# Kernel tuning notes

Measured on AMD Instinct MI355X. Metric: run time of the kernel, lower is better.

Reference implementation:

```python
import jax, jax.numpy as jnp
import numpy as np

K = 3
PAD = 1
K2 = K * K


def _deform_conv(x, offset, w, b):
    """torchvision-style DeformConv2d, stride=1, padding=1, kernel=3, dilation=1.
    x: [B,C,H,W]; offset: [B,2*K2,H,W] (per-tap (dy,dx) interleaved); w: [O,C,K,K]; b: [O].
    """
    B, C, H, W = x.shape
    # kernel tap offsets relative to center (padding=1 => taps at -1,0,1)
    ky = (jnp.arange(K) - PAD).astype(x.dtype)
    kx = (jnp.arange(K) - PAD).astype(x.dtype)
    ky = jnp.repeat(ky, K)   # [K2]
    kx = jnp.tile(kx, K)     # [K2]

    off = offset.reshape(B, K2, 2, H, W)
    # sampling coordinates: [B,K2,H,W]
    yy = off[:, :, 0] + ky[None, :, None, None] + jnp.arange(H, dtype=x.dtype)[None, None, :, None]
    xx = off[:, :, 1] + kx[None, :, None, None] + jnp.arange(W, dtype=x.dtype)[None, None, None, :]

    def sample_one(img, yb, xb):  # img [C,H,W]; yb,xb [K2,H,W]
        y0 = jnp.floor(yb)
        x0 = jnp.floor(xb)
        dy = yb - y0
        dx = xb - x0
        y0i = y0.astype(jnp.int32)
        x0i = x0.astype(jnp.int32)
        img_flat = img.reshape(C, -1)

        def gather(yi, xi):
            valid = (yi >= 0) & (yi < H) & (xi >= 0) & (xi < W)
            idx = jnp.clip(yi, 0, H - 1) * W + jnp.clip(xi, 0, W - 1)
            v = jnp.take(img_flat, idx.reshape(-1), axis=1).reshape(C, K2, H, W)
            return v * valid[None].astype(img.dtype)

        v00 = gather(y0i, x0i)
        v01 = gather(y0i, x0i + 1)
        v10 = gather(y0i + 1, x0i)
        v11 = gather(y0i + 1, x0i + 1)
        w00 = ((1 - dy) * (1 - dx))[None]
        w01 = ((1 - dy) * dx)[None]
        w10 = (dy * (1 - dx))[None]
        w11 = (dy * dx)[None]
        return v00 * w00 + v01 * w01 + v10 * w10 + v11 * w11  # [C,K2,H,W]

    samp = jax.vmap(sample_one)(x, yy, xx)  # [B,C,K2,H,W]
    wr = w.reshape(w.shape[0], C, K2)       # [O,C,K2]
    out = jnp.einsum('bckhw,ock->bohw', samp, wr)
    return out + b[None, :, None, None]


def setup_inputs() -> dict:
    key = jax.random.key(0)
    ks = jax.random.split(key, 8)
    B, Cin, H, W = 16, 256, 32, 32
    Ch, NC = 256, 1000
    fan1 = Cin * K2
    fan2 = Ch * K2
    return {
        'x': jax.random.normal(ks[0], (B, Cin, H, W), jnp.float32),
        'offset': jax.random.normal(ks[1], (B, 2 * K2, H, W), jnp.float32),
        'w1': jax.random.normal(ks[2], (Ch, Cin, K, K), jnp.float32) / np.sqrt(fan1),
        'b1': jnp.zeros((Ch,), jnp.float32),
        'w2': jax.random.normal(ks[3], (Ch, Ch, K, K), jnp.float32) / np.sqrt(fan2),
        'b2': jnp.zeros((Ch,), jnp.float32),
        'fc_w': jax.random.normal(ks[4], (NC, Ch), jnp.float32) / np.sqrt(Ch),
        'fc_b': jnp.zeros((NC,), jnp.float32),
    }


def reference(x, offset, w1, b1, w2, b2, fc_w, fc_b):
    h = jax.nn.relu(_deform_conv(x, offset, w1, b1))
    h = jax.nn.relu(_deform_conv(h, offset, w2, b2))
    pooled = h.mean(axis=(2, 3))            # adaptive_avg_pool2d to (1,1) then flatten
    return pooled @ fc_w.T + fc_b
```

## Files before the change

kernel.cpp:

```cpp
#include <hip/hip_runtime.h>

#define B_     16
#define C_     256
#define H_     32
#define W_     32
#define O_     256
#define K2_    9
#define HW_    1024
#define KTOT   2304
#define NPOS   16384
#define NCHUNK 288

typedef __bf16 bf16;
typedef __attribute__((ext_vector_type(8))) __bf16 bf16x8;
typedef __attribute__((ext_vector_type(4))) float  f32x4;

__device__ __forceinline__ void gload_lds16(const bf16* g, bf16* l) {
    __builtin_amdgcn_global_load_lds(
        (const __attribute__((address_space(1))) void*)g,
        (__attribute__((address_space(3))) void*)l, 16, 0, 0);
}

__device__ __forceinline__ float4 load4(const float* p, int t) {
    return ((const float4*)p)[t];
}
__device__ __forceinline__ float4 load4(const bf16* p, int t) {
    const ushort4 u = ((const ushort4*)p)[t];
    float4 f;
    f.x = __uint_as_float((unsigned)u.x << 16);
    f.y = __uint_as_float((unsigned)u.y << 16);
    f.z = __uint_as_float((unsigned)u.z << 16);
    f.w = __uint_as_float((unsigned)u.w << 16);
    return f;
}

__global__ __launch_bounds__(256) void prep_w(
    const float* __restrict__ w1, const float* __restrict__ w2,
    bf16* __restrict__ Wt1, bf16* __restrict__ Wt2,
    float* __restrict__ pooled)
{
    const int bx = blockIdx.x;
    const float* w  = (bx < 256) ? w1 : w2;
    bf16*      Wt   = (bx < 256) ? Wt1 : Wt2;
    const int o     = bx & 255;
    const int om    = o >> 7, o128 = o & 127;
    if (bx < 16) pooled[bx * 256 + threadIdx.x] = 0.f;
    for (int k = threadIdx.x; k < KTOT; k += 256) {
        const int cg  = k / 72;
        const int rem = k - cg * 72;
        const int tap = rem >> 3;
        const int cl  = rem & 7;
        const int c   = cg * 8 + cl;
        const int chunk = cg * 9 + tap;
        Wt[(((size_t)om * NCHUNK + chunk) * 128 + o128) * 8 + cl] =
            (bf16)w[((size_t)o * C_ + c) * K2_ + tap];
    }
}

template<typename T>
__global__ __launch_bounds__(256, 4) void sample_kernel(
    const T* __restrict__ src, size_t c_stride, size_t b_stride,
    const float* __restrict__ off,
    bf16* __restrict__ S)
{
    __shared__ float4 xs4[2][1152];

    const int tid = threadIdx.x;
    const int cg  = blockIdx.x & 31;
    const int rq  = (blockIdx.x >> 5) & 3;
    const int b   = blockIdx.x >> 7;

    #pragma unroll
    for (int h = 0; h < 2; ++h) {
        const T* base = src + b * b_stride + (size_t)(cg * 8 + h * 4) * c_stride;
        const float4 v0 = load4(base,                tid);
        const float4 v1 = load4(base + c_stride,     tid);
        const float4 v2 = load4(base + 2 * c_stride, tid);
        const float4 v3 = load4(base + 3 * c_stride, tid);
        const int p0 = 4 * tid;
        xs4[h][(p0    ) + ((p0    ) >> 3)] = make_float4(v0.x, v1.x, v2.x, v3.x);
        xs4[h][(p0 + 1) + ((p0 + 1) >> 3)] = make_float4(v0.y, v1.y, v2.y, v3.y);
        xs4[h][(p0 + 2) + ((p0 + 2) >> 3)] = make_float4(v0.z, v1.z, v2.z, v3.z);
        xs4[h][(p0 + 3) + ((p0 + 3) >> 3)] = make_float4(v0.w, v1.w, v2.w, v3.w);
    }

    const int pos = tid & 63;
    const int rt  = rq * 4 + (tid >> 6);
    const int y   = rt * 2 + (pos >> 5);
    const int x   = pos & 31;
    const float* offb = off + ((size_t)(b * 18) << 10) + (y << 5) + x;
    float dyo[9], dxo[9];
    #pragma unroll
    for (int k = 0; k < 9; ++k) {
        dyo[k] = offb[(size_t)(2 * k) << 10];
        dxo[k] = offb[((size_t)(2 * k) << 10) + 1024];
    }
    __syncthreads();

    const size_t tbase = ((size_t)(b * 16 + rt) * NCHUNK + cg * 9) * 64 * 8;
    #pragma unroll
    for (int tap = 0; tap < 9; ++tap) {
        const float yy = dyo[tap] + (float)(tap / 3 - 1) + (float)y;
        const float xx = dxo[tap] + (float)(tap % 3 - 1) + (float)x;
        const float fy0 = floorf(yy), fx0 = floorf(xx);
        const float dy = yy - fy0, dx = xx - fx0;
        const int iy0 = (int)fy0, ix0 = (int)fx0;
        const int iy1 = iy0 + 1,  ix1 = ix0 + 1;
        const bool vy0 = (iy0 >= 0) && (iy0 < H_);
        const bool vy1 = (iy1 >= 0) && (iy1 < H_);
        const bool vx0 = (ix0 >= 0) && (ix0 < W_);
        const bool vx1 = (ix1 >= 0) && (ix1 < W_);
        const int cy0 = min(max(iy0, 0), H_ - 1), cy1 = min(max(iy1, 0), H_ - 1);
        const int cx0 = min(max(ix0, 0), W_ - 1), cx1 = min(max(ix1, 0), W_ - 1);
        const int p00 = cy0 * W_ + cx0, p01 = cy0 * W_ + cx1;
        const int p10 = cy1 * W_ + cx0, p11 = cy1 * W_ + cx1;
        const float w00 = (vy0 && vx0) ? (1.f - dy) * (1.f - dx) : 0.f;
        const float w01 = (vy0 && vx1) ? (1.f - dy) * dx         : 0.f;
        const float w10 = (vy1 && vx0) ? dy * (1.f - dx)         : 0.f;
        const float w11 = (vy1 && vx1) ? dy * dx                 : 0.f;
        const int s0 = p00 + (p00 >> 3);
        const int s1 = p01 + (p01 >> 3);
        const int s2 = p10 + (p10 >> 3);
        const int s3 = p11 + (p11 >> 3);
        bf16x8 v;
        #pragma unroll
        for (int h = 0; h < 2; ++h) {
            const float4 a = xs4[h][s0], bb = xs4[h][s1];
            const float4 c = xs4[h][s2], d  = xs4[h][s3];
            v[h * 4 + 0] = (bf16)(w00 * a.x + w01 * bb.x + w10 * c.x + w11 * d.x);
            v[h * 4 + 1] = (bf16)(w00 * a.y + w01 * bb.y + w10 * c.y + w11 * d.y);
            v[h * 4 + 2] = (bf16)(w00 * a.z + w01 * bb.z + w10 * c.z + w11 * d.z);
            v[h * 4 + 3] = (bf16)(w00 * a.w + w01 * bb.w + w10 * c.w + w11 * d.w);
        }
        *(bf16x8*)(S + tbase + (size_t)tap * 64 * 8 + pos * 8) = v;
    }
}

template<bool POOL>
__global__ __launch_bounds__(256) void gemm_kernel(
    const bf16* __restrict__ A,
    const bf16* __restrict__ Bm,
    const float* __restrict__ bias,
    bf16* __restrict__ F,
    float* __restrict__ pooled)
{
    __shared__ bf16 Bl[2][4096];

    const int tid  = threadIdx.x;
    const int om   = blockIdx.x >> 8;
    const int pn   = blockIdx.x & 255;
    const int wave = tid >> 6, lane = tid & 63;
    const int wr   = wave >> 1, wc = wave & 1;
    const int l15  = lane & 15, l4 = lane >> 4;

    const bf16* Abase = A  + (size_t)om * NCHUNK * 128 * 8;
    const bf16* Bbase = Bm + (size_t)pn * NCHUNK * 64 * 8;

    f32x4 acc[4][2];
    #pragma unroll
    for (int m = 0; m < 4; ++m)
        #pragma unroll
        for (int n = 0; n < 2; ++n) acc[m][n] = (f32x4)0.f;

    #define STAGE_B(buf, kt)                                                  \
        do {                                                                  \
            _Pragma("unroll")                                                 \
            for (int i = 0; i < 2; ++i)                                       \
                gload_lds16(Bbase + (size_t)(kt) * 4096 + (i * 256 + tid) * 8,\
                            &Bl[buf][(i * 256 + wave * 64) * 8]);             \
        } while (0)

    STAGE_B(0, 0);
    __syncthreads();

    for (int kt = 0; kt < NCHUNK / 8; ++kt) {
        const int cur = kt & 1;
        if (kt < NCHUNK / 8 - 1) STAGE_B(cur ^ 1, kt + 1);

        #pragma unroll
        for (int ks = 0; ks < 2; ++ks) {
            const int cb = ks * 4 + l4;
            bf16x8 af[4], bq[2];
            #pragma unroll
            for (int m = 0; m < 4; ++m) {
                const int R = wr * 64 + m * 16 + l15;
                af[m] = *(const bf16x8*)(Abase +
                        (((size_t)kt * 8 + cb) * 128 + R) * 8);
            }
            #pragma unroll
            for (int n = 0; n < 2; ++n) {
                const int R = wc * 32 + n * 16 + l15;
                bq[n] = *(const bf16x8*)&Bl[cur][(cb * 64 + R) * 8];
            }
            #pragma unroll
            for (int m = 0; m < 4; ++m)
                #pragma unroll
                for (int n = 0; n < 2; ++n)
                    acc[m][n] = __builtin_amdgcn_mfma_f32_16x16x32_bf16(
                        af[m], bq[n], acc[m][n], 0, 0, 0);
        }
        __syncthreads();
    }
    #undef STAGE_B

    const int obase = om * 128 + wr * 64;
    if (!POOL) {
        #pragma unroll
        for (int m = 0; m < 4; ++m)
            #pragma unroll
            for (int j = 0; j < 4; ++j) {
                const int o  = obase + m * 16 + l4 * 4 + j;
                const float bb = bias[o];
                #pragma unroll
                for (int n = 0; n < 2; ++n) {
                    const int col = pn * 64 + wc * 32 + n * 16 + l15;
                    F[(size_t)o * NPOS + col] =
                        (bf16)fmaxf(acc[m][n][j] + bb, 0.f);
                }
            }
    } else {
        const int b = pn >> 4;
        #pragma unroll
        for (int m = 0; m < 4; ++m)
            #pragma unroll
            for (int j = 0; j < 4; ++j) {
                const int o  = obase + m * 16 + l4 * 4 + j;
                const float bb = bias[o];
                float s = fmaxf(acc[m][0][j] + bb, 0.f) +
                          fmaxf(acc[m][1][j] + bb, 0.f);
                s += __shfl_xor(s, 1);
                s += __shfl_xor(s, 2);
                s += __shfl_xor(s, 4);
                s += __shfl_xor(s, 8);
                if (l15 == 0)
                    atomicAdd(&pooled[b * 256 + o], s * (1.f / 1024.f));
            }
    }
}

__global__ __launch_bounds__(256) void fc_kernel(
    const float* __restrict__ pooled, const float* __restrict__ fw,
    const float* __restrict__ fb, float* __restrict__ out)
{
    __shared__ float pl[C_];
    const int b = blockIdx.x >> 2;
    const int q = blockIdx.x & 3;
    const int t = threadIdx.x;
    pl[t] = pooled[b * C_ + t];
    __syncthreads();
    const int n = q * 250 + t;
    if (t < 250) {
        const float4* wr = (const float4*)(fw + (size_t)n * C_);
        float s = 0.f;
        #pragma unroll 8
        for (int j = 0; j < C_ / 4; ++j) {
            const float4 v = wr[j];
            s += v.x * pl[4 * j] + v.y * pl[4 * j + 1] +
                 v.z * pl[4 * j + 2] + v.w * pl[4 * j + 3];
        }
        out[b * 1000 + n] = s + fb[n];
    }
}

extern "C" void kernel_launch(void* const* d_in, const int* in_sizes, int n_in,
                              void* d_out, int out_size, void* d_ws, size_t ws_size,
                              hipStream_t stream)
{
    const float* x   = (const float*)d_in[0];
    const float* off = (const float*)d_in[1];
    const float* w1  = (const float*)d_in[2];
    const float* b1  = (const float*)d_in[3];
    const float* w2  = (const float*)d_in[4];
    const float* b2  = (const float*)d_in[5];
    const float* fcw = (const float*)d_in[6];
    const float* fcb = (const float*)d_in[7];
    float* outp = (float*)d_out;

    bf16*  S      = (bf16*)d_ws;
    bf16*  F2     = S + (size_t)NPOS * KTOT;
    bf16*  Wt1    = F2 + (size_t)O_ * NPOS;
    bf16*  Wt2    = Wt1 + (size_t)O_ * KTOT;
    float* pooled = (float*)(Wt2 + (size_t)O_ * KTOT);

    prep_w<<<512, 256, 0, stream>>>(w1, w2, Wt1, Wt2, pooled);

    sample_kernel<float><<<2048, 256, 0, stream>>>(
        x, (size_t)HW_, (size_t)C_ * HW_, off, S);
    gemm_kernel<false><<<512, 256, 0, stream>>>(Wt1, S, b1, F2, nullptr);

    sample_kernel<bf16><<<2048, 256, 0, stream>>>(
        F2, (size_t)NPOS, (size_t)HW_, off, S);
    gemm_kernel<true><<<512, 256, 0, stream>>>(Wt2, S, b2, nullptr, pooled);

    fc_kernel<<<B_ * 4, 256, 0, stream>>>(pooled, fcw, fcb, outp);
}
```

Before: 221.8 us.

## Restructure deform-conv GEMM to per-wave 16x64 tiles with register double-buffering

The GEMM kernel stops staging the B operand through LDS with global_load_lds and block-wide barriers. Each wave now computes an independent 16x64 output tile, loading A and B fragments straight from global memory into registers, double-buffered across k-steps. The grid doubles to 1024 blocks for more parallelism. In exchange, each output tile is smaller, so operand reuse drops and global/L2 traffic per MFMA goes up.

```diff
diff --git a/kernel.cpp b/kernel.cpp
--- a/kernel.cpp
+++ b/kernel.cpp
@@ -14,12 +14,6 @@
 typedef __bf16 bf16;
 typedef __attribute__((ext_vector_type(8))) __bf16 bf16x8;
 typedef __attribute__((ext_vector_type(4))) float  f32x4;
-
-__device__ __forceinline__ void gload_lds16(const bf16* g, bf16* l) {
-    __builtin_amdgcn_global_load_lds(
-        (const __attribute__((address_space(1))) void*)g,
-        (__attribute__((address_space(3))) void*)l, 16, 0, 0);
-}
 
 __device__ __forceinline__ float4 load4(const float* p, int t) {
     return ((const float4*)p)[t];
@@ -144,97 +138,77 @@
     bf16* __restrict__ F,
     float* __restrict__ pooled)
 {
-    __shared__ bf16 Bl[2][4096];
-
     const int tid  = threadIdx.x;
-    const int om   = blockIdx.x >> 8;
-    const int pn   = blockIdx.x & 255;
     const int wave = tid >> 6, lane = tid & 63;
-    const int wr   = wave >> 1, wc = wave & 1;
     const int l15  = lane & 15, l4 = lane >> 4;
-
-    const bf16* Abase = A  + (size_t)om * NCHUNK * 128 * 8;
-    const bf16* Bbase = Bm + (size_t)pn * NCHUNK * 64 * 8;
-
-    f32x4 acc[4][2];
-    #pragma unroll
-    for (int m = 0; m < 4; ++m)
-        #pragma unroll
-        for (int n = 0; n < 2; ++n) acc[m][n] = (f32x4)0.f;
-
-    #define STAGE_B(buf, kt)                                                  \
+    const int og   = (blockIdx.x & 3) * 4 + wave;
+    const int pn   = blockIdx.x >> 2;
+    const int om   = og >> 3;
+
+    const bf16* Ab = A + (size_t)om * (NCHUNK * 1024)
+                       + ((size_t)((og & 7) * 16 + l15)) * 8;
+    const bf16* Bb = Bm + (size_t)pn * (NCHUNK * 512) + (size_t)l15 * 8;
+
+    f32x4 acc[4];
+    #pragma unroll
+    for (int n = 0; n < 4; ++n) acc[n] = (f32x4)0.f;
+
+    bf16x8 aC, bC0, bC1, bC2, bC3;
+    bf16x8 aN, bN0, bN1, bN2, bN3;
+
+    #define LD(ksg, a, b0, b1, b2, b3)                                        \
         do {                                                                  \
-            _Pragma("unroll")                                                 \
-            for (int i = 0; i < 2; ++i)                                       \
-                gload_lds16(Bbase + (size_t)(kt) * 4096 + (i * 256 + tid) * 8,\
-                            &Bl[buf][(i * 256 + wave * 64) * 8]);             \
+            const size_t co = (size_t)((ksg) * 4 + l4);                       \
+            a  = *(const bf16x8*)(Ab + co * 1024);                            \
+            b0 = *(const bf16x8*)(Bb + co * 512);                             \
+            b1 = *(const bf16x8*)(Bb + co * 512 + 128);                       \
+            b2 = *(const bf16x8*)(Bb + co * 512 + 256);                       \
+            b3 = *(const bf16x8*)(Bb + co * 512 + 384);                       \
         } while (0)
 
-    STAGE_B(0, 0);
-    __syncthreads();
-
-    for (int kt = 0; kt < NCHUNK / 8; ++kt) {
-        const int cur = kt & 1;
-        if (kt < NCHUNK / 8 - 1) STAGE_B(cur ^ 1, kt + 1);
-
-        #pragma unroll
-        for (int ks = 0; ks < 2; ++ks) {
-            const int cb = ks * 4 + l4;
-            bf16x8 af[4], bq[2];
-            #pragma unroll
-            for (int m = 0; m < 4; ++m) {
-                const int R = wr * 64 + m * 16 + l15;
-                af[m] = *(const bf16x8*)(Abase +
-                        (((size_t)kt * 8 + cb) * 128 + R) * 8);
-            }
-            #pragma unroll
-            for (int n = 0; n < 2; ++n) {
-                const int R = wc * 32 + n * 16 + l15;
-                bq[n] = *(const bf16x8*)&Bl[cur][(cb * 64 + R) * 8];
-            }
-            #pragma unroll
-            for (int m = 0; m < 4; ++m)
-                #pragma unroll
-                for (int n = 0; n < 2; ++n)
-                    acc[m][n] = __builtin_amdgcn_mfma_f32_16x16x32_bf16(
-                        af[m], bq[n], acc[m][n], 0, 0, 0);
-        }
-        __syncthreads();
-    }
-    #undef STAGE_B
-
-    const int obase = om * 128 + wr * 64;
+    #define MM(a, b0, b1, b2, b3)                                             \
+        do {                                                                  \
+            acc[0] = __builtin_amdgcn_mfma_f32_16x16x32_bf16(a, b0, acc[0], 0, 0, 0); \
+            acc[1] = __builtin_amdgcn_mfma_f32_16x16x32_bf16(a, b1, acc[1], 0, 0, 0); \
+            acc[2] = __builtin_amdgcn_mfma_f32_16x16x32_bf16(a, b2, acc[2], 0, 0, 0); \
+            acc[3] = __builtin_amdgcn_mfma_f32_16x16x32_bf16(a, b3, acc[3], 0, 0, 0); \
+        } while (0)
+
+    LD(0, aC, bC0, bC1, bC2, bC3);
+    for (int ksg = 0; ksg < 72; ksg += 2) {
+        LD(ksg + 1, aN, bN0, bN1, bN2, bN3);
+        MM(aC, bC0, bC1, bC2, bC3);
+        if (ksg + 2 < 72) LD(ksg + 2, aC, bC0, bC1, bC2, bC3);
+        MM(aN, bN0, bN1, bN2, bN3);
+    }
+    #undef LD
+    #undef MM
+
+    const int ob = og * 16 + l4 * 4;
     if (!POOL) {
         #pragma unroll
-        for (int m = 0; m < 4; ++m)
+        for (int j = 0; j < 4; ++j) {
+            const float bb = bias[ob + j];
             #pragma unroll
-            for (int j = 0; j < 4; ++j) {
-                const int o  = obase + m * 16 + l4 * 4 + j;
-                const float bb = bias[o];
-                #pragma unroll
-                for (int n = 0; n < 2; ++n) {
-                    const int col = pn * 64 + wc * 32 + n * 16 + l15;
-                    F[(size_t)o * NPOS + col] =
-                        (bf16)fmaxf(acc[m][n][j] + bb, 0.f);
-                }
-            }
+            for (int n = 0; n < 4; ++n)
+                F[(size_t)(ob + j) * NPOS + pn * 64 + n * 16 + l15] =
+                    (bf16)fmaxf(acc[n][j] + bb, 0.f);
+        }
     } else {
         const int b = pn >> 4;
         #pragma unroll
-        for (int m = 0; m < 4; ++m)
+        for (int j = 0; j < 4; ++j) {
+            const float bb = bias[ob + j];
+            float s = 0.f;
             #pragma unroll
-            for (int j = 0; j < 4; ++j) {
-                const int o  = obase + m * 16 + l4 * 4 + j;
-                const float bb = bias[o];
-                float s = fmaxf(acc[m][0][j] + bb, 0.f) +
-                          fmaxf(acc[m][1][j] + bb, 0.f);
-                s += __shfl_xor(s, 1);
-                s += __shfl_xor(s, 2);
-                s += __shfl_xor(s, 4);
-                s += __shfl_xor(s, 8);
-                if (l15 == 0)
-                    atomicAdd(&pooled[b * 256 + o], s * (1.f / 1024.f));
-            }
+            for (int n = 0; n < 4; ++n) s += fmaxf(acc[n][j] + bb, 0.f);
+            s += __shfl_xor(s, 1);
+            s += __shfl_xor(s, 2);
+            s += __shfl_xor(s, 4);
+            s += __shfl_xor(s, 8);
+            if (l15 == 0)
+                atomicAdd(&pooled[b * 256 + ob + j], s * (1.f / 1024.f));
+        }
     }
 }
 
@@ -286,11 +260,11 @@
 
     sample_kernel<float><<<2048, 256, 0, stream>>>(
         x, (size_t)HW_, (size_t)C_ * HW_, off, S);
-    gemm_kernel<false><<<512, 256, 0, stream>>>(Wt1, S, b1, F2, nullptr);
+    gemm_kernel<false><<<1024, 256, 0, stream>>>(Wt1, S, b1, F2, nullptr);
 
     sample_kernel<bf16><<<2048, 256, 0, stream>>>(
         F2, (size_t)NPOS, (size_t)HW_, off, S);
-    gemm_kernel<true><<<512, 256, 0, stream>>>(Wt2, S, b2, nullptr, pooled);
+    gemm_kernel<true><<<1024, 256, 0, stream>>>(Wt2, S, b2, nullptr, pooled);
 
     fc_kernel<<<B_ * 4, 256, 0, stream>>>(pooled, fcw, fcb, outp);
 }
```

After: 232.4 us. 4.8% more time.
